# Kernel tuning notes

Hardware: AMD Instinct MI355X
Metric: run time of the kernel (lower is better)

The kernel has to match this reference:

```python
import jax, jax.numpy as jnp
import numpy as np

S, B, H = 2048, 1, 1024
N_HEADS = 16
HEAD_DIM = H // N_HEADS
E, K, F = 8, 2, 2048  # experts, top_k, ffn_hidden
EPS = 1e-5


def layernorm(x, w, b):
    mu = jnp.mean(x, axis=-1, keepdims=True)
    var = jnp.mean(jnp.square(x - mu), axis=-1, keepdims=True)
    return (x - mu) * jax.lax.rsqrt(var + EPS) * w + b


def setup_inputs() -> dict:
    key = jax.random.key(0)
    ks = jax.random.split(key, 8)
    std = 0.02
    return {
        "x": jax.random.normal(ks[0], (S, B, H), dtype=jnp.float32),
        "ln1_w": jnp.ones((H,), jnp.float32),
        "ln1_b": jnp.zeros((H,), jnp.float32),
        "in_proj_w": jax.random.normal(ks[1], (3 * H, H), jnp.float32) * std,
        "in_proj_b": jnp.zeros((3 * H,), jnp.float32),
        "out_proj_w": jax.random.normal(ks[2], (H, H), jnp.float32) * std,
        "out_proj_b": jnp.zeros((H,), jnp.float32),
        "ln2_w": jnp.ones((H,), jnp.float32),
        "ln2_b": jnp.zeros((H,), jnp.float32),
        "router_w": jax.random.normal(ks[3], (E, H), jnp.float32) * std,
        "w1": jax.random.normal(ks[4], (E, H, F), jnp.float32) * std,
        "w2": jax.random.normal(ks[5], (E, F, H), jnp.float32) * std,
    }


def reference(x, ln1_w, ln1_b, in_proj_w, in_proj_b, out_proj_w, out_proj_b,
              ln2_w, ln2_b, router_w, w1, w2):
    s, b, h = x.shape
    # ---- causal self-attention (nn.MultiheadAttention math) ----
    hn = layernorm(x, ln1_w, ln1_b)
    qkv = hn @ in_proj_w.T + in_proj_b          # [S,B,3H]
    q, k, v = jnp.split(qkv, 3, axis=-1)
    q = q.reshape(s, b, N_HEADS, HEAD_DIM)
    k = k.reshape(s, b, N_HEADS, HEAD_DIM)
    v = v.reshape(s, b, N_HEADS, HEAD_DIM)
    scores = jnp.einsum('sbnd,tbnd->bnst', q, k) / np.sqrt(HEAD_DIM)
    causal = jnp.tril(jnp.ones((s, s), bool))
    scores = jnp.where(causal[None, None], scores, -jnp.inf)
    probs = jax.nn.softmax(scores, axis=-1)
    attn = jnp.einsum('bnst,tbnd->sbnd', probs, v).reshape(s, b, h)
    attn = attn @ out_proj_w.T + out_proj_b
    x1 = x + attn
    # ---- dMoE FFN: router softmax -> top-k gates -> expert GELU MLP ----
    hn2 = layernorm(x1, ln2_w, ln2_b).reshape(s * b, h)   # tokens [T,H]
    logits = hn2 @ router_w.T                              # [T,E]
    rp = jax.nn.softmax(logits, axis=-1)
    topw, topi = jax.lax.top_k(rp, K)                      # [T,K]
    gates = jnp.sum(jax.nn.one_hot(topi, E, dtype=hn2.dtype) * topw[..., None], axis=1)  # [T,E]
    hmid = jax.nn.gelu(jnp.einsum('th,ehf->tef', hn2, w1), approximate=False)  # [T,E,F]
    y = jnp.einsum('tef,efh->th', hmid * gates[:, :, None], w2)                # [T,H]
    return x1 + y.reshape(s, b, h)
```

## Files before the change

### kernel.cpp

```cpp
#include <hip/hip_runtime.h>

#define SL 2048
#define HID 1024
#define NHEAD 16
#define HD 64
#define NEXP 8
#define FF 2048
#define MAXTILE 40
#define MAXROWS (MAXTILE * 128)
#define CPAD 32

typedef short bf16x8 __attribute__((ext_vector_type(8)));
typedef float f32x4 __attribute__((ext_vector_type(4)));
typedef unsigned u32x4 __attribute__((ext_vector_type(4)));

__device__ __forceinline__ unsigned short f2bf(float f) {
  unsigned u = __builtin_bit_cast(unsigned, f);
  u += 0x7fffu + ((u >> 16) & 1u);
  return (unsigned short)(u >> 16);
}

__device__ __forceinline__ void gload16(const void* g, void* l) {
  __builtin_amdgcn_global_load_lds((const __attribute__((address_space(1))) void*)g,
                                   (__attribute__((address_space(3))) void*)l,
                                   16, 0, 0);
}

__device__ __forceinline__ void xcd_remap(int& bx, int& by) {
  const int nx = gridDim.x;
  const int nwg = nx * gridDim.y;
  const int L = by * nx + bx;
  const int per = nwg >> 3;
  const int Lp = (L & 7) * per + (L >> 3);
  bx = Lp % nx;
  by = Lp / nx;
}


#define PIPE_WAIT(i, NT)                                                     \
  if ((i) == (NT) - 1)                                                       \
    asm volatile("s_waitcnt vmcnt(0) lgkmcnt(0)" ::: "memory");              \
  else                                                                       \
    asm volatile("s_waitcnt vmcnt(4) lgkmcnt(0)" ::: "memory");              \
  __builtin_amdgcn_s_barrier();

#define GEMM_FRAGS_MFMA(CC)                                                  \
  bf16x8 af[4], bfr[4];                                                      \
  _Pragma("unroll")                                                          \
  for (int mt = 0; mt < 4; mt++)                                             \
    af[mt] = *reinterpret_cast<const bf16x8*>(                               \
        &Asm[CC][(wm + mt * 16 + la) * 32 + lk]);                            \
  _Pragma("unroll")                                                          \
  for (int nt = 0; nt < 4; nt++)                                             \
    bfr[nt] = *reinterpret_cast<const bf16x8*>(                              \
        &Bsm[CC][(wn + nt * 16 + la) * 32 + lk]);                            \
  _Pragma("unroll")                                                          \
  for (int mt = 0; mt < 4; mt++)                                             \
    _Pragma("unroll")                                                        \
    for (int nt = 0; nt < 4; nt++)                                           \
      acc[mt][nt] =                                                          \
          __builtin_amdgcn_mfma_f32_16x16x32_bf16(af[mt], bfr[nt], acc[mt][nt], 0, 0, 0);

#define PIPE_ROT()                                                           \
  cc = (cc == 2) ? 0 : cc + 1;                                               \
  cs = (cs == 2) ? 0 : cs + 1;

template <int MODE>
__global__ __launch_bounds__(256) void gemm_bt(
    const unsigned short* __restrict__ A, const unsigned short* __restrict__ Bt,
    int M, int N, int Kstride, int Kloop,
    const float* __restrict__ bias,
    float* __restrict__ outf,
    unsigned short* __restrict__ q_out, unsigned short* __restrict__ k_out,
    unsigned short* __restrict__ vt_out)
{
  __shared__ unsigned short Asm[3][128 * 32];
  __shared__ unsigned short Bsm[3][128 * 32];
  int bx = blockIdx.x, by = blockIdx.y;
  xcd_remap(bx, by);
  const int tid = threadIdx.x;
  const int wave = tid >> 6;
  const int lane = tid & 63;
  const int m0 = by * 128;
  const int n0 = bx * 128;
  const int koff = blockIdx.z * Kloop;
  const int wm = (wave >> 1) * 64;
  const int wn = (wave & 1) * 64;
  const int la = lane & 15;
  const int lk = (lane >> 4) * 8;

  f32x4 acc[4][4] = {};

  const int srow = tid >> 2;
  const int skoff = (tid & 3) * 8;
  const unsigned short* Ag = A + (size_t)(m0 + srow) * Kstride + koff + skoff;
  const unsigned short* Bg = Bt + (size_t)(n0 + srow) * Kstride + koff + skoff;

  auto stage = [&](int s, int k0) {
    gload16(Ag + k0, &Asm[s][wave * 512]);
    gload16(Ag + (size_t)64 * Kstride + k0, &Asm[s][2048 + wave * 512]);
    gload16(Bg + k0, &Bsm[s][wave * 512]);
    gload16(Bg + (size_t)64 * Kstride + k0, &Bsm[s][2048 + wave * 512]);
  };

  stage(0, 0);
  stage(1, 32);
  const int NT = Kloop >> 5;
  int cc = 0, cs = 2;
  for (int i = 0; i < NT; ++i) {
    PIPE_WAIT(i, NT)
    if (i + 2 < NT) stage(cs, (i + 2) << 5);
    GEMM_FRAGS_MFMA(cc)
    PIPE_ROT()
  }

  const int lg = lane >> 4;
#pragma unroll
  for (int mt = 0; mt < 4; mt++) {
#pragma unroll
    for (int nt = 0; nt < 4; nt++) {
#pragma unroll
      for (int r = 0; r < 4; r++) {
        const int row = m0 + wm + mt * 16 + lg * 4 + r;
        const int col = n0 + wn + nt * 16 + la;
        float v = acc[mt][nt][r];
        if (MODE == 0) {
          v += bias[col];
          const int hh = (col & 1023) >> 6;
          const int dd = col & 63;
          const unsigned short bv = f2bf(v);
          if (col < 1024)
            q_out[(size_t)hh * SL * HD + (size_t)row * HD + dd] = bv;
          else if (col < 2048)
            k_out[(size_t)hh * SL * HD + (size_t)row * HD + dd] = bv;
          else
            vt_out[(size_t)hh * HD * SL + (size_t)dd * SL + row] = bv;
        } else {
          outf[(size_t)blockIdx.z * SL * HID + (size_t)row * HID + col] = v;
        }
      }
    }
  }
}

__global__ __launch_bounds__(256) void gemm_moe1(
    const unsigned short* __restrict__ A, const unsigned short* __restrict__ w1t,
    const int* __restrict__ perm, const float* __restrict__ gateg,
    const int* __restrict__ texp, const int* __restrict__ trow,
    unsigned short* __restrict__ hmidg)
{
  __shared__ unsigned short Asm[3][128 * 32];
  __shared__ unsigned short Bsm[3][128 * 32];
  int bx = blockIdx.x, by = blockIdx.y;
  xcd_remap(bx, by);
  const int e = texp[by];
  if (e < 0) return;
  const int row0 = trow[by];
  const int tid = threadIdx.x;
  const int wave = tid >> 6;
  const int lane = tid & 63;
  const int n0 = bx * 128;
  const int wm = (wave >> 1) * 64;
  const int wn = (wave & 1) * 64;
  const int la = lane & 15;
  const int lk = (lane >> 4) * 8;
  f32x4 acc[4][4] = {};

  const int srow = tid >> 2;
  const int skoff = (tid & 3) * 8;
  const int p0 = perm[row0 + srow];
  const int p1 = perm[row0 + 64 + srow];
  const unsigned short* Ag0 = A + (size_t)(p0 < 0 ? 0 : (p0 >> 1)) * HID + skoff;
  const unsigned short* Ag1 = A + (size_t)(p1 < 0 ? 0 : (p1 >> 1)) * HID + skoff;
  const unsigned short* Bg = w1t + (size_t)e * HID * FF + (size_t)(n0 + srow) * HID + skoff;

  auto stage = [&](int s, int k0) {
    gload16(Ag0 + k0, &Asm[s][wave * 512]);
    gload16(Ag1 + k0, &Asm[s][2048 + wave * 512]);
    gload16(Bg + k0, &Bsm[s][wave * 512]);
    gload16(Bg + (size_t)64 * HID + k0, &Bsm[s][2048 + wave * 512]);
  };

  stage(0, 0);
  stage(1, 32);
  const int NT = HID >> 5;
  int cc = 0, cs = 2;
  for (int i = 0; i < NT; ++i) {
    PIPE_WAIT(i, NT)
    if (i + 2 < NT) stage(cs, (i + 2) << 5);
    GEMM_FRAGS_MFMA(cc)
    PIPE_ROT()
  }

  const int lg = lane >> 4;
#pragma unroll
  for (int mt = 0; mt < 4; mt++) {
    float gr[4];
#pragma unroll
    for (int r = 0; r < 4; r++) gr[r] = gateg[row0 + wm + mt * 16 + lg * 4 + r];
#pragma unroll
    for (int nt = 0; nt < 4; nt++) {
#pragma unroll
      for (int r = 0; r < 4; r++) {
        const int grow = row0 + wm + mt * 16 + lg * 4 + r;
        const int col = n0 + wn + nt * 16 + la;
        const float v = acc[mt][nt][r];
        const float g = 0.5f * v * (1.0f + erff(v * 0.70710678118f));
        hmidg[(size_t)grow * FF + col] = f2bf(g * gr[r]);
      }
    }
  }
}

__global__ __launch_bounds__(256) void gemm_moe2(
    const unsigned short* __restrict__ A, const unsigned short* __restrict__ w2t,
    const int* __restrict__ perm,
    const int* __restrict__ texp, const int* __restrict__ trow,
    float* __restrict__ ybuf)
{
  __shared__ unsigned short Asm[3][128 * 32];
  __shared__ unsigned short Bsm[3][128 * 32];
  int bx = blockIdx.x, by = blockIdx.y;
  xcd_remap(bx, by);
  const int e = texp[by];
  if (e < 0) return;
  const int row0 = trow[by];
  const int tid = threadIdx.x;
  const int wave = tid >> 6;
  const int lane = tid & 63;
  const int n0 = bx * 128;
  const int koff = blockIdx.z * (FF / 2);
  const int wm = (wave >> 1) * 64;
  const int wn = (wave & 1) * 64;
  const int la = lane & 15;
  const int lk = (lane >> 4) * 8;
  f32x4 acc[4][4] = {};

  const int srow = tid >> 2;
  const int skoff = (tid & 3) * 8;
  const unsigned short* Ag = A + (size_t)(row0 + srow) * FF + koff + skoff;
  const unsigned short* Bg = w2t + (size_t)e * FF * HID + (size_t)(n0 + srow) * FF + koff + skoff;

  auto stage = [&](int s, int k0) {
    gload16(Ag + k0, &Asm[s][wave * 512]);
    gload16(Ag + (size_t)64 * FF + k0, &Asm[s][2048 + wave * 512]);
    gload16(Bg + k0, &Bsm[s][wave * 512]);
    gload16(Bg + (size_t)64 * FF + k0, &Bsm[s][2048 + wave * 512]);
  };

  stage(0, 0);
  stage(1, 32);
  const int NT = (FF / 2) >> 5;
  int cc = 0, cs = 2;
  for (int i = 0; i < NT; ++i) {
    PIPE_WAIT(i, NT)
    if (i + 2 < NT) stage(cs, (i + 2) << 5);
    GEMM_FRAGS_MFMA(cc)
    PIPE_ROT()
  }

  const int lg = lane >> 4;
#pragma unroll
  for (int mt = 0; mt < 4; mt++) {
    int pr[4];
#pragma unroll
    for (int r = 0; r < 4; r++) pr[r] = perm[row0 + wm + mt * 16 + lg * 4 + r];
#pragma unroll
    for (int nt = 0; nt < 4; nt++) {
#pragma unroll
      for (int r = 0; r < 4; r++) {
        const int p = pr[r];
        if (p >= 0) {
          const int col = n0 + wn + nt * 16 + la;
          ybuf[(size_t)(blockIdx.z * 2 + (p & 1)) * SL * HID + (size_t)(p >> 1) * HID + col] =
              acc[mt][nt][r];
        }
      }
    }
  }
}

__global__ __launch_bounds__(256) void ln_kernel(
    const float* __restrict__ x, const float* __restrict__ w, const float* __restrict__ b,
    unsigned short* __restrict__ ob, float* __restrict__ of)
{
  const int row = blockIdx.x;
  const int tid = threadIdx.x;
  const float4 v = *reinterpret_cast<const float4*>(&x[(size_t)row * HID + tid * 4]);
  float s = v.x + v.y + v.z + v.w;
  float q = v.x * v.x + v.y * v.y + v.z * v.z + v.w * v.w;
  for (int off = 32; off > 0; off >>= 1) {
    s += __shfl_down(s, off);
    q += __shfl_down(q, off);
  }
  __shared__ float ps[4], pq[4];
  const int wave = tid >> 6, lane = tid & 63;
  if (lane == 0) { ps[wave] = s; pq[wave] = q; }
  __syncthreads();
  s = ps[0] + ps[1] + ps[2] + ps[3];
  q = pq[0] + pq[1] + pq[2] + pq[3];
  const float mu = s * (1.0f / HID);
  const float inv = rsqrtf(q * (1.0f / HID) - mu * mu + 1e-5f);
  const int i = tid * 4;
  const float4 wv = *reinterpret_cast<const float4*>(&w[i]);
  const float4 bv = *reinterpret_cast<const float4*>(&b[i]);
  const float o0 = (v.x - mu) * inv * wv.x + bv.x;
  const float o1 = (v.y - mu) * inv * wv.y + bv.y;
  const float o2 = (v.z - mu) * inv * wv.z + bv.z;
  const float o3 = (v.w - mu) * inv * wv.w + bv.w;
  ushort4 u; u.x = f2bf(o0); u.y = f2bf(o1); u.z = f2bf(o2); u.w = f2bf(o3);
  *reinterpret_cast<ushort4*>(&ob[(size_t)row * HID + i]) = u;
  if (of) {
    float4 o; o.x = o0; o.y = o1; o.z = o2; o.w = o3;
    *reinterpret_cast<float4*>(&of[(size_t)row * HID + i]) = o;
  }
}

__global__ __launch_bounds__(256) void transpose_bf16(
    const float* __restrict__ in, unsigned short* __restrict__ out, int R, int C)
{
  __shared__ float t[64][65];
  const size_t base = (size_t)blockIdx.z * R * C;
  const int r0 = blockIdx.y * 64, c0 = blockIdx.x * 64;
  const int tid = threadIdx.x;
#pragma unroll
  for (int it = 0; it < 4; it++) {
    const int idx = it * 256 + tid;
    const int r = idx >> 4, c4 = (idx & 15) * 4;
    const float4 v = *reinterpret_cast<const float4*>(&in[base + (size_t)(r0 + r) * C + c0 + c4]);
    t[r][c4] = v.x; t[r][c4 + 1] = v.y; t[r][c4 + 2] = v.z; t[r][c4 + 3] = v.w;
  }
  __syncthreads();
#pragma unroll
  for (int it = 0; it < 4; it++) {
    const int idx = it * 256 + tid;
    const int c = idx >> 4, r4 = (idx & 15) * 4;
    ushort4 u;
    u.x = f2bf(t[r4][c]); u.y = f2bf(t[r4 + 1][c]);
    u.z = f2bf(t[r4 + 2][c]); u.w = f2bf(t[r4 + 3][c]);
    *reinterpret_cast<ushort4*>(&out[base + (size_t)(c0 + c) * R + r0 + r4]) = u;
  }
}

__global__ __launch_bounds__(256) void conv_bf16(
    const float4* __restrict__ in, ushort4* __restrict__ out, int n4)
{
  const int i = blockIdx.x * 256 + threadIdx.x;
  if (i < n4) {
    const float4 v = in[i];
    ushort4 u; u.x = f2bf(v.x); u.y = f2bf(v.y); u.z = f2bf(v.z); u.w = f2bf(v.w);
    out[i] = u;
  }
}

__global__ __launch_bounds__(256) void router_kernel(
    const float* __restrict__ hn2f, const float* __restrict__ rw,
    int* __restrict__ ti, float* __restrict__ tg, int* __restrict__ cnt)
{
  __shared__ float wlds[NEXP * HID];
  __shared__ int lcnt[NEXP];
  const int tid = threadIdx.x;
#pragma unroll
  for (int i = 0; i < 8; i++)
    *reinterpret_cast<float4*>(&wlds[i * 1024 + tid * 4]) =
        *reinterpret_cast<const float4*>(&rw[i * 1024 + tid * 4]);
  if (tid < NEXP) lcnt[tid] = 0;
  __syncthreads();

  const int wave = tid >> 6, lane = tid & 63;
#pragma unroll 1
  for (int k = 0; k < 4; k++) {
    const int t = blockIdx.x * 16 + wave * 4 + k;
    float4 xr[4];
#pragma unroll
    for (int c = 0; c < 4; c++)
      xr[c] = *reinterpret_cast<const float4*>(&hn2f[(size_t)t * HID + c * 256 + lane * 4]);
    float p[NEXP];
#pragma unroll
    for (int e = 0; e < NEXP; e++) {
      float s = 0.f;
#pragma unroll
      for (int c = 0; c < 4; c++) {
        const float4 wv = *reinterpret_cast<const float4*>(&wlds[e * 1024 + c * 256 + lane * 4]);
        s += xr[c].x * wv.x + xr[c].y * wv.y + xr[c].z * wv.z + xr[c].w * wv.w;
      }
      s += __shfl_xor(s, 32);
      s += __shfl_xor(s, 16);
      s += __shfl_xor(s, 8);
      s += __shfl_xor(s, 4);
      s += __shfl_xor(s, 2);
      s += __shfl_xor(s, 1);
      p[e] = s;
    }
    if (lane == 0) {
      float mx = p[0];
#pragma unroll
      for (int e = 1; e < NEXP; e++) mx = fmaxf(mx, p[e]);
      float Z = 0.f;
#pragma unroll
      for (int e = 0; e < NEXP; e++) { p[e] = expf(p[e] - mx); Z += p[e]; }
      const float invZ = 1.f / Z;
      int i1 = 0;
#pragma unroll
      for (int e = 1; e < NEXP; e++) if (p[e] > p[i1]) i1 = e;
      int i2 = (i1 == 0) ? 1 : 0;
#pragma unroll
      for (int e = 0; e < NEXP; e++) if (e != i1 && p[e] > p[i2]) i2 = e;
      ti[2 * t] = i1; ti[2 * t + 1] = i2;
      tg[2 * t] = p[i1] * invZ; tg[2 * t + 1] = p[i2] * invZ;
      atomicAdd(&lcnt[i1], 1);
      atomicAdd(&lcnt[i2], 1);
    }
  }
  __syncthreads();
  if (tid < NEXP && lcnt[tid] > 0) atomicAdd(&cnt[tid * CPAD], lcnt[tid]);
}

__global__ void scan_kernel(const int* __restrict__ cnt, int* __restrict__ poff,
                            int* __restrict__ texp, int* __restrict__ trow)
{
  if (threadIdx.x == 0 && blockIdx.x == 0) {
    int off = 0, nt = 0;
    for (int e = 0; e < NEXP; e++) {
      poff[e] = off;
      const int c = cnt[e * CPAD];
      const int ntl = (c + 127) >> 7;
      for (int i = 0; i < ntl; i++) { texp[nt] = e; trow[nt] = off + i * 128; nt++; }
      off += ntl * 128;
    }
    for (int i = nt; i < MAXTILE; i++) { texp[i] = -1; trow[i] = 0; }
  }
}

__global__ __launch_bounds__(256) void build_kernel(
    const int* __restrict__ ti, const float* __restrict__ tg,
    const int* __restrict__ poff, int* __restrict__ fill,
    int* __restrict__ perm, float* __restrict__ gateg)
{
  __shared__ int lcnt[NEXP], lbase[NEXP];
  const int tid = threadIdx.x;
  if (tid < NEXP) lcnt[tid] = 0;
  __syncthreads();
  const int t = blockIdx.x * 256 + tid;
  int e0 = ti[2 * t], e1 = ti[2 * t + 1];
  int l0 = atomicAdd(&lcnt[e0], 1);
  int l1 = atomicAdd(&lcnt[e1], 1);
  __syncthreads();
  if (tid < NEXP) lbase[tid] = (lcnt[tid] > 0) ? atomicAdd(&fill[tid * CPAD], lcnt[tid]) : 0;
  __syncthreads();
  int pos0 = poff[e0] + lbase[e0] + l0;
  int pos1 = poff[e1] + lbase[e1] + l1;
  perm[pos0] = 2 * t;
  gateg[pos0] = tg[2 * t];
  perm[pos1] = 2 * t + 1;
  gateg[pos1] = tg[2 * t + 1];
}

__global__ __launch_bounds__(256) void combine_x1(
    const float4* __restrict__ x, const float* __restrict__ bias,
    const float4* __restrict__ p0, const float4* __restrict__ p1,
    float4* __restrict__ x1)
{
  const int i = blockIdx.x * 256 + threadIdx.x;
  const int col = (i * 4) & (HID - 1);
  const float4 bv = *reinterpret_cast<const float4*>(&bias[col]);
  const float4 a = x[i], b = p0[i], c = p1[i];
  float4 o;
  o.x = a.x + bv.x + b.x + c.x;
  o.y = a.y + bv.y + b.y + c.y;
  o.z = a.z + bv.z + b.z + c.z;
  o.w = a.w + bv.w + b.w + c.w;
  x1[i] = o;
}

__global__ __launch_bounds__(256) void final_add(
    const float4* __restrict__ x1, const float4* __restrict__ y0,
    const float4* __restrict__ y1, const float4* __restrict__ y2,
    const float4* __restrict__ y3, float4* __restrict__ out)
{
  const int i = blockIdx.x * 256 + threadIdx.x;
  const float4 a = x1[i], b = y0[i], c = y1[i], d = y2[i], e = y3[i];
  float4 o;
  o.x = a.x + b.x + c.x + d.x + e.x;
  o.y = a.y + b.y + c.y + d.y + e.y;
  o.z = a.z + b.z + c.z + d.z + e.z;
  o.w = a.w + b.w + c.w + d.w + e.w;
  out[i] = o;
}

#define SC2 0.1803368801111204f
#define PPITCH 20
__global__ __launch_bounds__(512) void attn_kernel(
    const unsigned short* __restrict__ qb, const unsigned short* __restrict__ kb,
    const unsigned short* __restrict__ vtb, unsigned short* __restrict__ attn)
{
  const int h = blockIdx.y;
  const int tid = threadIdx.x;
  const int wave = tid >> 6, lane = tid & 63;
  const int grp = wave >> 2;
  const int w4 = wave & 3;
  const int la = lane & 15, lg = lane >> 4;
  const int la7 = la & 7;
  __shared__ unsigned short Kt[2][2][64 * 64];
  __shared__ unsigned short Vt[2][2][64 * 64];
  __shared__ unsigned plds[8 * 32 * PPITCH];
  const unsigned short* qh = qb + (size_t)h * SL * HD;
  const unsigned short* kh = kb + (size_t)h * SL * HD;
  const unsigned short* vh = vtb + (size_t)h * HD * SL;
  unsigned* pu = &plds[wave * 32 * PPITCH];

  const int sr_lo = w4 * 8 + (lane >> 3);
  const int ss = lane & 7;

  auto stageKV = [&](int t, int buf) {
    const int kvb = t * 64;
#pragma unroll
    for (int j = 0; j < 2; j++) {
      const int row = j * 32 + sr_lo;
      const int s = ss ^ (row & 7);
      gload16(kh + (size_t)(kvb + row) * HD + s * 8, &Kt[grp][buf][j * 2048 + w4 * 512]);
      gload16(vh + (size_t)row * SL + kvb + s * 8, &Vt[grp][buf][j * 2048 + w4 * 512]);
    }
  };

  for (int half = 0; half < 2; half++) {
    const int qt = half ? (31 - blockIdx.x) : blockIdx.x;
    const int m0 = qt * 64 + w4 * 16;
    const int T = qt + 1;
    const int S = (T + 1) >> 1;
    const int q = m0 + la;

    bf16x8 aq0 = *reinterpret_cast<const bf16x8*>(&qh[(size_t)(m0 + la) * HD + lg * 8]);
    bf16x8 aq1 = *reinterpret_cast<const bf16x8*>(&qh[(size_t)(m0 + la) * HD + 32 + lg * 8]);

    f32x4 oacc[4] = {};
    float mrun = -1e30f, lrun = 0.f;

    if (grp < T) stageKV(grp, 0);
    __syncthreads();
    int cur = 0;

    for (int s = 0; s < S; s++) {
      const int tmy = 2 * s + grp;
      if (tmy + 2 < T) stageKV(tmy + 2, cur ^ 1);
      if (tmy < T) {
        const int kv0 = tmy * 64;
        const unsigned short* Kb = Kt[grp][cur];
        const unsigned short* Vb = Vt[grp][cur];

        f32x4 sac[4] = {};
#pragma unroll
        for (int nt = 0; nt < 4; nt++) {
          const int row = nt * 16 + la;
          bf16x8 b0 = *reinterpret_cast<const bf16x8*>(&Kb[row * 64 + ((lg ^ la7) << 3)]);
          bf16x8 b1 = *reinterpret_cast<const bf16x8*>(&Kb[row * 64 + (((4 + lg) ^ la7) << 3)]);
          sac[nt] = __builtin_amdgcn_mfma_f32_16x16x32_bf16(b0, aq0, sac[nt], 0, 0, 0);
          sac[nt] = __builtin_amdgcn_mfma_f32_16x16x32_bf16(b1, aq1, sac[nt], 0, 0, 0);
        }
        float sv[4][4];
        const bool diag = (tmy == qt);
#pragma unroll
        for (int nt = 0; nt < 4; nt++)
#pragma unroll
          for (int r = 0; r < 4; r++) {
            float xs = sac[nt][r] * SC2;
            if (diag && (kv0 + nt * 16 + lg * 4 + r) > q) xs = -1e30f;
            sv[nt][r] = xs;
          }
        float pm = fmaxf(fmaxf(sv[0][0], sv[0][1]), fmaxf(sv[0][2], sv[0][3]));
#pragma unroll
        for (int nt = 1; nt < 4; nt++)
          pm = fmaxf(pm, fmaxf(fmaxf(sv[nt][0], sv[nt][1]), fmaxf(sv[nt][2], sv[nt][3])));
        pm = fmaxf(pm, __shfl_xor(pm, 16));
        pm = fmaxf(pm, __shfl_xor(pm, 32));
        const float mn = fmaxf(mrun, pm);
        float rs = 0.f;
#pragma unroll
        for (int nt = 0; nt < 4; nt++)
#pragma unroll
          for (int r = 0; r < 4; r++) {
            const float pe = exp2f(sv[nt][r] - mn);
            sv[nt][r] = pe;
            rs += pe;
          }
        rs += __shfl_xor(rs, 16);
        rs += __shfl_xor(rs, 32);
        if (__ballot(pm > mrun) != 0ULL) {
          const float al = exp2f(mrun - mn);
#pragma unroll
          for (int dt = 0; dt < 4; dt++)
#pragma unroll
            for (int r = 0; r < 4; r++) oacc[dt][r] *= al;
          lrun = lrun * al + rs;
          mrun = mn;
        } else {
          lrun += rs;
        }
#pragma unroll
        for (int nt = 0; nt < 4; nt++)
#pragma unroll
          for (int rp = 0; rp < 2; rp++) {
            unsigned pk;
            asm("v_cvt_pk_bf16_f32 %0, %1, %2"
                : "=v"(pk) : "v"(sv[nt][rp * 2]), "v"(sv[nt][rp * 2 + 1]));
            pu[(nt * 8 + lg * 2 + rp) * PPITCH + la] = pk;
          }
        asm volatile("s_waitcnt lgkmcnt(0)" ::: "memory");
        __builtin_amdgcn_sched_barrier(0);
        u32x4 w0, w1;
#pragma unroll
        for (int jj = 0; jj < 4; jj++) {
          w0[jj] = pu[(lg * 4 + jj) * PPITCH + la];
          w1[jj] = pu[(16 + lg * 4 + jj) * PPITCH + la];
        }
        const bf16x8 pa0 = __builtin_bit_cast(bf16x8, w0);
        const bf16x8 pa1 = __builtin_bit_cast(bf16x8, w1);
#pragma unroll
        for (int dt = 0; dt < 4; dt++) {
          const int row = dt * 16 + la;
          bf16x8 v0 = *reinterpret_cast<const bf16x8*>(&Vb[row * 64 + ((lg ^ la7) << 3)]);
          bf16x8 v1 = *reinterpret_cast<const bf16x8*>(&Vb[row * 64 + (((4 + lg) ^ la7) << 3)]);
          oacc[dt] = __builtin_amdgcn_mfma_f32_16x16x32_bf16(v0, pa0, oacc[dt], 0, 0, 0);
          oacc[dt] = __builtin_amdgcn_mfma_f32_16x16x32_bf16(v1, pa1, oacc[dt], 0, 0, 0);
        }
      }
      __syncthreads();
      cur ^= 1;
    }

    float* xb = (float*)&Kt[0][0][0];
    float* mlb = (float*)&Vt[0][0][0];
    if (grp == 1) {
#pragma unroll
      for (int dt = 0; dt < 4; dt++)
#pragma unroll
        for (int r = 0; r < 4; r++)
          xb[w4 * 1024 + (dt * 16 + lg * 4 + r) * 16 + la] = oacc[dt][r];
      if (lg == 0) {
        mlb[w4 * 32 + la * 2] = mrun;
        mlb[w4 * 32 + la * 2 + 1] = lrun;
      }
    }
    __syncthreads();
    if (grp == 0) {
      const float m1 = mlb[w4 * 32 + la * 2];
      const float l1 = mlb[w4 * 32 + la * 2 + 1];
      const float mm = fmaxf(mrun, m1);
      const float a0 = exp2f(mrun - mm);
      const float a1 = exp2f(m1 - mm);
      const float linv = 1.0f / (lrun * a0 + l1 * a1);
#pragma unroll
      for (int dt = 0; dt < 4; dt++) {
        ushort4 u;
        float o0 = (oacc[dt][0] * a0 + xb[w4 * 1024 + (dt * 16 + lg * 4 + 0) * 16 + la] * a1) * linv;
        float o1 = (oacc[dt][1] * a0 + xb[w4 * 1024 + (dt * 16 + lg * 4 + 1) * 16 + la] * a1) * linv;
        float o2 = (oacc[dt][2] * a0 + xb[w4 * 1024 + (dt * 16 + lg * 4 + 2) * 16 + la] * a1) * linv;
        float o3 = (oacc[dt][3] * a0 + xb[w4 * 1024 + (dt * 16 + lg * 4 + 3) * 16 + la] * a1) * linv;
        u.x = f2bf(o0); u.y = f2bf(o1); u.z = f2bf(o2); u.w = f2bf(o3);
        *reinterpret_cast<ushort4*>(&attn[(size_t)q * HID + h * HD + dt * 16 + lg * 4]) = u;
      }
    }
    __syncthreads();
  }
}

extern "C" void kernel_launch(void* const* d_in, const int* in_sizes, int n_in,
                              void* d_out, int out_size, void* d_ws, size_t ws_size,
                              hipStream_t stream)
{
  const float* x          = (const float*)d_in[0];
  const float* ln1_w      = (const float*)d_in[1];
  const float* ln1_b      = (const float*)d_in[2];
  const float* in_proj_w  = (const float*)d_in[3];
  const float* in_proj_b  = (const float*)d_in[4];
  const float* out_proj_w = (const float*)d_in[5];
  const float* out_proj_b = (const float*)d_in[6];
  const float* ln2_w      = (const float*)d_in[7];
  const float* ln2_b      = (const float*)d_in[8];
  const float* router_w   = (const float*)d_in[9];
  const float* w1         = (const float*)d_in[10];
  const float* w2         = (const float*)d_in[11];
  float* out = (float*)d_out;

  char* ws = (char*)d_ws;
  size_t off = 0;
  auto alloc = [&](size_t bytes) -> void* {
    void* p = ws + off;
    off += (bytes + 255) & ~(size_t)255;
    return p;
  };
  unsigned short* hn_b   = (unsigned short*)alloc((size_t)SL * HID * 2);
  unsigned short* ipw_b  = (unsigned short*)alloc((size_t)3 * HID * HID * 2);
  unsigned short* opw_b  = (unsigned short*)alloc((size_t)HID * HID * 2);
  unsigned short* qb     = (unsigned short*)alloc((size_t)SL * HID * 2);
  unsigned short* kb     = (unsigned short*)alloc((size_t)SL * HID * 2);
  unsigned short* vtb    = (unsigned short*)alloc((size_t)SL * HID * 2);
  unsigned short* attn_b = (unsigned short*)alloc((size_t)SL * HID * 2);
  float*          x1     = (float*)alloc((size_t)SL * HID * 4);
  float*          pbuf   = (float*)alloc((size_t)2 * SL * HID * 4);
  unsigned short* hn2_b  = (unsigned short*)alloc((size_t)SL * HID * 2);
  float*          hn2_f  = (float*)alloc((size_t)SL * HID * 4);
  unsigned short* w1t    = (unsigned short*)alloc((size_t)NEXP * HID * FF * 2);
  unsigned short* w2t    = (unsigned short*)alloc((size_t)NEXP * HID * FF * 2);
  unsigned short* hmidg  = (unsigned short*)alloc((size_t)MAXROWS * FF * 2);
  float*          ybuf   = (float*)alloc((size_t)4 * SL * HID * 4);
  int*            ti     = (int*)alloc((size_t)SL * 2 * 4);
  float*          tg     = (float*)alloc((size_t)SL * 2 * 4);
  int*            perm   = (int*)alloc((size_t)MAXROWS * 4);
  float*          gateg  = (float*)alloc((size_t)MAXROWS * 4);
  int*            cnt    = (int*)alloc(NEXP * CPAD * 4);
  int*            fill   = (int*)alloc(NEXP * CPAD * 4);
  int*            poff   = (int*)alloc(64 * 4);
  int*            texp   = (int*)alloc(64 * 4);
  int*            trow   = (int*)alloc(64 * 4);

  const dim3 blk(256);

  hipMemsetAsync(cnt, 0, NEXP * CPAD * 4, stream);
  hipMemsetAsync(fill, 0, NEXP * CPAD * 4, stream);
  hipMemsetAsync(perm, 0xFF, (size_t)MAXROWS * 4, stream);
  hipMemsetAsync(gateg, 0, (size_t)MAXROWS * 4, stream);

  conv_bf16<<<(3 * HID * HID / 4 + 255) / 256, blk, 0, stream>>>(
      (const float4*)in_proj_w, (ushort4*)ipw_b, 3 * HID * HID / 4);
  conv_bf16<<<(HID * HID / 4 + 255) / 256, blk, 0, stream>>>(
      (const float4*)out_proj_w, (ushort4*)opw_b, HID * HID / 4);
  transpose_bf16<<<dim3(FF / 64, HID / 64, NEXP), blk, 0, stream>>>(w1, w1t, HID, FF);
  transpose_bf16<<<dim3(HID / 64, FF / 64, NEXP), blk, 0, stream>>>(w2, w2t, FF, HID);

  ln_kernel<<<SL, blk, 0, stream>>>(x, ln1_w, ln1_b, hn_b, nullptr);

  gemm_bt<0><<<dim3(3 * HID / 128, SL / 128), blk, 0, stream>>>(
      hn_b, ipw_b, SL, 3 * HID, HID, HID,
      in_proj_b, nullptr, qb, kb, vtb);

  attn_kernel<<<dim3(16, NHEAD), dim3(512), 0, stream>>>(qb, kb, vtb, attn_b);

  gemm_bt<2><<<dim3(HID / 128, SL / 128, 2), blk, 0, stream>>>(
      attn_b, opw_b, SL, HID, HID, HID / 2,
      nullptr, pbuf, nullptr, nullptr, nullptr);
  combine_x1<<<SL * HID / 1024, blk, 0, stream>>>(
      (const float4*)x, out_proj_b, (const float4*)pbuf,
      (const float4*)(pbuf + (size_t)SL * HID), (float4*)x1);

  ln_kernel<<<SL, blk, 0, stream>>>(x1, ln2_w, ln2_b, hn2_b, hn2_f);

  router_kernel<<<SL / 16, blk, 0, stream>>>(hn2_f, router_w, ti, tg, cnt);
  scan_kernel<<<1, 64, 0, stream>>>(cnt, poff, texp, trow);
  build_kernel<<<SL / 256, blk, 0, stream>>>(ti, tg, poff, fill, perm, gateg);

  gemm_moe1<<<dim3(FF / 128, MAXTILE), blk, 0, stream>>>(
      hn2_b, w1t, perm, gateg, texp, trow, hmidg);
  gemm_moe2<<<dim3(HID / 128, MAXTILE, 2), blk, 0, stream>>>(
      hmidg, w2t, perm, texp, trow, ybuf);

  final_add<<<SL * HID / 1024, blk, 0, stream>>>(
      (const float4*)x1, (const float4*)ybuf,
      (const float4*)(ybuf + (size_t)SL * HID),
      (const float4*)(ybuf + (size_t)2 * SL * HID),
      (const float4*)(ybuf + (size_t)3 * SL * HID),
      (float4*)out);
}
```

Baseline: 273.8 us.

## Fuse residual combine with LayerNorm, merge weight-prep launches, raise MFMA priority

```diff
diff --git a/kernel.cpp b/kernel.cpp
--- a/kernel.cpp
+++ b/kernel.cpp
@@ -54,12 +54,14 @@
   for (int nt = 0; nt < 4; nt++)                                             \
     bfr[nt] = *reinterpret_cast<const bf16x8*>(                              \
         &Bsm[CC][(wn + nt * 16 + la) * 32 + lk]);                            \
+  __builtin_amdgcn_s_setprio(1);                                             \
   _Pragma("unroll")                                                          \
   for (int mt = 0; mt < 4; mt++)                                             \
     _Pragma("unroll")                                                        \
     for (int nt = 0; nt < 4; nt++)                                           \
       acc[mt][nt] =                                                          \
-          __builtin_amdgcn_mfma_f32_16x16x32_bf16(af[mt], bfr[nt], acc[mt][nt], 0, 0, 0);
+          __builtin_amdgcn_mfma_f32_16x16x32_bf16(af[mt], bfr[nt], acc[mt][nt], 0, 0, 0); \
+  __builtin_amdgcn_s_setprio(0);
 
 #define PIPE_ROT()                                                           \
   cc = (cc == 2) ? 0 : cc + 1;                                               \
@@ -282,7 +284,7 @@
 
 __global__ __launch_bounds__(256) void ln_kernel(
     const float* __restrict__ x, const float* __restrict__ w, const float* __restrict__ b,
-    unsigned short* __restrict__ ob, float* __restrict__ of)
+    unsigned short* __restrict__ ob)
 {
   const int row = blockIdx.x;
   const int tid = threadIdx.x;
@@ -304,30 +306,81 @@
   const int i = tid * 4;
   const float4 wv = *reinterpret_cast<const float4*>(&w[i]);
   const float4 bv = *reinterpret_cast<const float4*>(&b[i]);
+  ushort4 u;
+  u.x = f2bf((v.x - mu) * inv * wv.x + bv.x);
+  u.y = f2bf((v.y - mu) * inv * wv.y + bv.y);
+  u.z = f2bf((v.z - mu) * inv * wv.z + bv.z);
+  u.w = f2bf((v.w - mu) * inv * wv.w + bv.w);
+  *reinterpret_cast<ushort4*>(&ob[(size_t)row * HID + i]) = u;
+}
+
+__global__ __launch_bounds__(256) void combine_ln(
+    const float4* __restrict__ x, const float* __restrict__ bias,
+    const float4* __restrict__ p0, const float4* __restrict__ p1,
+    float4* __restrict__ x1,
+    const float* __restrict__ w, const float* __restrict__ b,
+    unsigned short* __restrict__ ob, float* __restrict__ of)
+{
+  const int row = blockIdx.x;
+  const int tid = threadIdx.x;
+  const int i4 = row * 256 + tid;
+  const int i = tid * 4;
+  const float4 bv0 = *reinterpret_cast<const float4*>(&bias[i]);
+  const float4 a = x[i4], c = p0[i4], d = p1[i4];
+  float4 v;
+  v.x = a.x + bv0.x + c.x + d.x;
+  v.y = a.y + bv0.y + c.y + d.y;
+  v.z = a.z + bv0.z + c.z + d.z;
+  v.w = a.w + bv0.w + c.w + d.w;
+  x1[i4] = v;
+  float s = v.x + v.y + v.z + v.w;
+  float q = v.x * v.x + v.y * v.y + v.z * v.z + v.w * v.w;
+  for (int off = 32; off > 0; off >>= 1) {
+    s += __shfl_down(s, off);
+    q += __shfl_down(q, off);
+  }
+  __shared__ float ps[4], pq[4];
+  const int wave = tid >> 6, lane = tid & 63;
+  if (lane == 0) { ps[wave] = s; pq[wave] = q; }
+  __syncthreads();
+  s = ps[0] + ps[1] + ps[2] + ps[3];
+  q = pq[0] + pq[1] + pq[2] + pq[3];
+  const float mu = s * (1.0f / HID);
+  const float inv = rsqrtf(q * (1.0f / HID) - mu * mu + 1e-5f);
+  const float4 wv = *reinterpret_cast<const float4*>(&w[i]);
+  const float4 bv = *reinterpret_cast<const float4*>(&b[i]);
   const float o0 = (v.x - mu) * inv * wv.x + bv.x;
   const float o1 = (v.y - mu) * inv * wv.y + bv.y;
   const float o2 = (v.z - mu) * inv * wv.z + bv.z;
   const float o3 = (v.w - mu) * inv * wv.w + bv.w;
   ushort4 u; u.x = f2bf(o0); u.y = f2bf(o1); u.z = f2bf(o2); u.w = f2bf(o3);
   *reinterpret_cast<ushort4*>(&ob[(size_t)row * HID + i]) = u;
-  if (of) {
-    float4 o; o.x = o0; o.y = o1; o.z = o2; o.w = o3;
-    *reinterpret_cast<float4*>(&of[(size_t)row * HID + i]) = o;
-  }
-}
-
-__global__ __launch_bounds__(256) void transpose_bf16(
-    const float* __restrict__ in, unsigned short* __restrict__ out, int R, int C)
+  float4 o; o.x = o0; o.y = o1; o.z = o2; o.w = o3;
+  *reinterpret_cast<float4*>(&of[(size_t)row * HID + i]) = o;
+}
+
+__global__ __launch_bounds__(256) void transpose_all(
+    const float* __restrict__ w1, const float* __restrict__ w2,
+    unsigned short* __restrict__ w1t, unsigned short* __restrict__ w2t)
 {
   __shared__ float t[64][65];
-  const size_t base = (size_t)blockIdx.z * R * C;
-  const int r0 = blockIdx.y * 64, c0 = blockIdx.x * 64;
+  const int z = blockIdx.z;
+  const float* in;
+  unsigned short* out;
+  int R, C, r0, c0;
+  if (z < 8) {
+    in = w1 + (size_t)z * HID * FF;  out = w1t + (size_t)z * HID * FF;
+    R = HID; C = FF;  r0 = blockIdx.y * 64;  c0 = blockIdx.x * 64;
+  } else {
+    in = w2 + (size_t)(z - 8) * FF * HID;  out = w2t + (size_t)(z - 8) * FF * HID;
+    R = FF; C = HID;  r0 = blockIdx.x * 64;  c0 = blockIdx.y * 64;
+  }
   const int tid = threadIdx.x;
 #pragma unroll
   for (int it = 0; it < 4; it++) {
     const int idx = it * 256 + tid;
     const int r = idx >> 4, c4 = (idx & 15) * 4;
-    const float4 v = *reinterpret_cast<const float4*>(&in[base + (size_t)(r0 + r) * C + c0 + c4]);
+    const float4 v = *reinterpret_cast<const float4*>(&in[(size_t)(r0 + r) * C + c0 + c4]);
     t[r][c4] = v.x; t[r][c4 + 1] = v.y; t[r][c4 + 2] = v.z; t[r][c4 + 3] = v.w;
   }
   __syncthreads();
@@ -338,18 +391,23 @@
     ushort4 u;
     u.x = f2bf(t[r4][c]); u.y = f2bf(t[r4 + 1][c]);
     u.z = f2bf(t[r4 + 2][c]); u.w = f2bf(t[r4 + 3][c]);
-    *reinterpret_cast<ushort4*>(&out[base + (size_t)(c0 + c) * R + r0 + r4]) = u;
-  }
-}
-
-__global__ __launch_bounds__(256) void conv_bf16(
-    const float4* __restrict__ in, ushort4* __restrict__ out, int n4)
+    *reinterpret_cast<ushort4*>(&out[(size_t)(c0 + c) * R + r0 + r4]) = u;
+  }
+}
+
+__global__ __launch_bounds__(256) void conv_bf16_2(
+    const float4* __restrict__ a, const float4* __restrict__ b,
+    ushort4* __restrict__ oa, ushort4* __restrict__ ob, int na4, int nb4)
 {
   const int i = blockIdx.x * 256 + threadIdx.x;
-  if (i < n4) {
-    const float4 v = in[i];
+  if (i < na4) {
+    const float4 v = a[i];
     ushort4 u; u.x = f2bf(v.x); u.y = f2bf(v.y); u.z = f2bf(v.z); u.w = f2bf(v.w);
-    out[i] = u;
+    oa[i] = u;
+  } else if (i - na4 < nb4) {
+    const float4 v = b[i - na4];
+    ushort4 u; u.x = f2bf(v.x); u.y = f2bf(v.y); u.z = f2bf(v.z); u.w = f2bf(v.w);
+    ob[i - na4] = u;
   }
 }
 
@@ -456,23 +514,6 @@
   gateg[pos1] = tg[2 * t + 1];
 }
 
-__global__ __launch_bounds__(256) void combine_x1(
-    const float4* __restrict__ x, const float* __restrict__ bias,
-    const float4* __restrict__ p0, const float4* __restrict__ p1,
-    float4* __restrict__ x1)
-{
-  const int i = blockIdx.x * 256 + threadIdx.x;
-  const int col = (i * 4) & (HID - 1);
-  const float4 bv = *reinterpret_cast<const float4*>(&bias[col]);
-  const float4 a = x[i], b = p0[i], c = p1[i];
-  float4 o;
-  o.x = a.x + bv.x + b.x + c.x;
-  o.y = a.y + bv.y + b.y + c.y;
-  o.z = a.z + bv.z + b.z + c.z;
-  o.w = a.w + bv.w + b.w + c.w;
-  x1[i] = o;
-}
-
 __global__ __launch_bounds__(256) void final_add(
     const float4* __restrict__ x1, const float4* __restrict__ y0,
     const float4* __restrict__ y1, const float4* __restrict__ y2,
@@ -549,6 +590,7 @@
         const unsigned short* Vb = Vt[grp][cur];
 
         f32x4 sac[4] = {};
+        __builtin_amdgcn_s_setprio(1);
 #pragma unroll
         for (int nt = 0; nt < 4; nt++) {
           const int row = nt * 16 + la;
@@ -557,6 +599,7 @@
           sac[nt] = __builtin_amdgcn_mfma_f32_16x16x32_bf16(b0, aq0, sac[nt], 0, 0, 0);
           sac[nt] = __builtin_amdgcn_mfma_f32_16x16x32_bf16(b1, aq1, sac[nt], 0, 0, 0);
         }
+        __builtin_amdgcn_s_setprio(0);
         float sv[4][4];
         const bool diag = (tmy == qt);
 #pragma unroll
@@ -615,6 +658,7 @@
         }
         const bf16x8 pa0 = __builtin_bit_cast(bf16x8, w0);
         const bf16x8 pa1 = __builtin_bit_cast(bf16x8, w1);
+        __builtin_amdgcn_s_setprio(1);
 #pragma unroll
         for (int dt = 0; dt < 4; dt++) {
           const int row = dt * 16 + la;
@@ -623,6 +667,7 @@
           oacc[dt] = __builtin_amdgcn_mfma_f32_16x16x32_bf16(v0, pa0, oacc[dt], 0, 0, 0);
           oacc[dt] = __builtin_amdgcn_mfma_f32_16x16x32_bf16(v1, pa1, oacc[dt], 0, 0, 0);
         }
+        __builtin_amdgcn_s_setprio(0);
       }
       __syncthreads();
       cur ^= 1;
@@ -721,14 +766,12 @@
   hipMemsetAsync(perm, 0xFF, (size_t)MAXROWS * 4, stream);
   hipMemsetAsync(gateg, 0, (size_t)MAXROWS * 4, stream);
 
-  conv_bf16<<<(3 * HID * HID / 4 + 255) / 256, blk, 0, stream>>>(
-      (const float4*)in_proj_w, (ushort4*)ipw_b, 3 * HID * HID / 4);
-  conv_bf16<<<(HID * HID / 4 + 255) / 256, blk, 0, stream>>>(
-      (const float4*)out_proj_w, (ushort4*)opw_b, HID * HID / 4);
-  transpose_bf16<<<dim3(FF / 64, HID / 64, NEXP), blk, 0, stream>>>(w1, w1t, HID, FF);
-  transpose_bf16<<<dim3(HID / 64, FF / 64, NEXP), blk, 0, stream>>>(w2, w2t, FF, HID);
-
-  ln_kernel<<<SL, blk, 0, stream>>>(x, ln1_w, ln1_b, hn_b, nullptr);
+  conv_bf16_2<<<4096, blk, 0, stream>>>(
+      (const float4*)in_proj_w, (const float4*)out_proj_w,
+      (ushort4*)ipw_b, (ushort4*)opw_b, 3 * HID * HID / 4, HID * HID / 4);
+  transpose_all<<<dim3(32, 16, 16), blk, 0, stream>>>(w1, w2, w1t, w2t);
+
+  ln_kernel<<<SL, blk, 0, stream>>>(x, ln1_w, ln1_b, hn_b);
 
   gemm_bt<0><<<dim3(3 * HID / 128, SL / 128), blk, 0, stream>>>(
       hn_b, ipw_b, SL, 3 * HID, HID, HID,
@@ -739,11 +782,11 @@
   gemm_bt<2><<<dim3(HID / 128, SL / 128, 2), blk, 0, stream>>>(
       attn_b, opw_b, SL, HID, HID, HID / 2,
       nullptr, pbuf, nullptr, nullptr, nullptr);
-  combine_x1<<<SL * HID / 1024, blk, 0, stream>>>(
+
+  combine_ln<<<SL, blk, 0, stream>>>(
       (const float4*)x, out_proj_b, (const float4*)pbuf,
-      (const float4*)(pbuf + (size_t)SL * HID), (float4*)x1);
-
-  ln_kernel<<<SL, blk, 0, stream>>>(x1, ln2_w, ln2_b, hn2_b, hn2_f);
+      (const float4*)(pbuf + (size_t)SL * HID), (float4*)x1,
+      ln2_w, ln2_b, hn2_b, hn2_f);
 
   router_kernel<<<SL / 16, blk, 0, stream>>>(hn2_f, router_w, ti, tg, cnt);
   scan_kernel<<<1, 64, 0, stream>>>(cnt, poff, texp, trow);
```

Result: faster. 263.4 us (-3.8%).
